# Optimization experiments

Hardware: AMD Instinct MI355X
Metric: run time of the kernel (lower is better)

## Reference

```python
import jax, jax.numpy as jnp
import numpy as np

N_HEADS = 16
HEAD_SIZE = 64
N_EMBD = N_HEADS * HEAD_SIZE  # 1024
B, T = 4, 2048


def setup_inputs() -> dict:
    key = jax.random.key(0)
    kx, kq, kk, kv, kp = jax.random.split(key, 5)
    s = 1.0 / np.sqrt(N_EMBD)
    return {
        "x": jax.random.normal(kx, (B, T, N_EMBD), dtype=jnp.float32),
        "Wq": jax.random.normal(kq, (N_EMBD, N_HEADS * HEAD_SIZE), dtype=jnp.float32) * s,
        "Wk": jax.random.normal(kk, (N_EMBD, N_HEADS * HEAD_SIZE), dtype=jnp.float32) * s,
        "Wv": jax.random.normal(kv, (N_EMBD, N_HEADS * HEAD_SIZE), dtype=jnp.float32) * s,
        "Wp": jax.random.normal(kp, (N_HEADS * HEAD_SIZE, N_EMBD), dtype=jnp.float32) * s,
    }


def reference(x, Wq, Wk, Wv, Wp):
    Bb, Tt, C = x.shape
    H, hs = N_HEADS, HEAD_SIZE
    # QKV projections (no bias), split heads: (B, H, T, hs)
    q = (x @ Wq).reshape(Bb, Tt, H, hs).transpose(0, 2, 1, 3)
    k = (x @ Wk).reshape(Bb, Tt, H, hs).transpose(0, 2, 1, 3)
    v = (x @ Wv).reshape(Bb, Tt, H, hs).transpose(0, 2, 1, 3)
    scores = jnp.einsum("bhqd,bhkd->bhqk", q, k) / np.sqrt(hs).astype(np.float32)
    causal = jnp.tril(jnp.ones((Tt, Tt), dtype=bool))
    scores = jnp.where(causal, scores, -jnp.inf)
    attn = jax.nn.softmax(scores, axis=-1)  # dropout p=0 -> identity
    o = jnp.einsum("bhqk,bhkd->bhqd", attn, v)  # (B, H, T, hs)
    # Faithfully replicate torch's view/transpose/view sequence:
    o = o.reshape(Bb, Tt, H * hs)          # raw reshape of (B,H,T,hs) buffer
    o = jnp.swapaxes(o, 1, 2)               # (B, H*hs, T)
    o = o.reshape(Bb, Tt, H * hs)           # contiguous().view
    return o @ Wp
```

## Files before the change

### kernel.cpp

```cpp
#include <hip/hip_runtime.h>

typedef unsigned short ush;
typedef unsigned int u32;
typedef __attribute__((ext_vector_type(4))) float f32x4;
typedef __attribute__((ext_vector_type(2))) u32 u32x2;
typedef __attribute__((ext_vector_type(8))) short short8;
typedef __attribute__((ext_vector_type(8))) ush ushx8;
typedef __attribute__((ext_vector_type(4))) ush ushx4;

#define GAS __attribute__((address_space(1)))
#define LAS __attribute__((address_space(3)))

__device__ __forceinline__ void gl_lds16(const void* g, void* l) {
  __builtin_amdgcn_global_load_lds((const GAS void*)g, (LAS void*)l, 16, 0, 0);
}

__device__ __forceinline__ ush f2bf(float f) {
  union { float f; unsigned int u; } x; x.f = f;
  unsigned int r = x.u + 0x7fffu + ((x.u >> 16) & 1u);
  return (ush)(r >> 16);
}
__device__ __forceinline__ u32 fbits(float f) {
  union { float f; u32 u; } x; x.f = f; return x.u;
}

#define NEG_BIG (-1.0e4f)
#define SCL 0.18033688f

__device__ __forceinline__ int kkey(int row) { return ((row & 3) + (row >> 2)) & 3; }

__global__ __launch_bounds__(256) void k_prep(
    const float* __restrict__ X, const float* __restrict__ W0,
    const float* __restrict__ W1, const float* __restrict__ W2,
    const float* __restrict__ W3, ush* __restrict__ Xb, ush* __restrict__ Wt) {
  __shared__ ush Ts[64][72];
  const int bx = blockIdx.x;
  if (bx < 4096) {
    int idx = bx * 256 + threadIdx.x;
    int base = idx * 8;
    f32x4 a = *(const f32x4*)(X + base);
    f32x4 b = *(const f32x4*)(X + base + 4);
    ushx8 o;
#pragma unroll
    for (int q = 0; q < 4; ++q) { o[q] = f2bf(a[q]); o[4 + q] = f2bf(b[q]); }
    *(ushx8*)(Xb + base) = o;
    return;
  }
  const int bid = bx - 4096;
  const int z = bid >> 8;
  const int k0 = (bid & 15) * 64, n0 = ((bid >> 4) & 15) * 64;
  const float* W = (z == 0) ? W0 : (z == 1) ? W1 : (z == 2) ? W2 : W3;
  ush* Ot = Wt + (size_t)z * 1048576;
  const int rr = threadIdx.x >> 4, cc = threadIdx.x & 15;
#pragma unroll
  for (int i = 0; i < 4; ++i) {
    int row = i * 16 + rr;
    f32x4 v = *(const f32x4*)(W + (size_t)(k0 + row) * 1024 + n0 + cc * 4);
#pragma unroll
    for (int q = 0; q < 4; ++q) Ts[row][cc * 4 + q] = f2bf(v[q]);
  }
  __syncthreads();
#pragma unroll
  for (int i = 0; i < 4; ++i) {
    int n = i * 16 + rr;
    ushx4 o;
#pragma unroll
    for (int q = 0; q < 4; ++q) o[q] = Ts[cc * 4 + q][n];
    *(ushx4*)(Ot + (size_t)(n0 + n) * 1024 + k0 + cc * 4) = o;
  }
}

__global__ __launch_bounds__(512, 2) void k_gemm_qkv(
    const ush* __restrict__ X, const ush* __restrict__ Wt,
    ush* __restrict__ QKV, ush* __restrict__ Vtg) {
  __shared__ __align__(16) ush sm[36864];
  const int tid = threadIdx.x;
  const int w = tid >> 6, l = tid & 63, lr = l & 15, lg = l >> 4;
  const int wm = w >> 2, wn = w & 3;
  const int mt = blockIdx.x, nt = blockIdx.y;
  const int which = nt >> 3, n0 = (nt & 7) * 128;
  const ush* Ag = X + (size_t)mt * 256 * 1024;
  const ush* Bg = Wt + (size_t)which * 1048576 + (size_t)n0 * 1024;
  int aoff[2], boff;
  {
#pragma unroll
    for (int it = 0; it < 2; ++it) {
      int ch = it * 512 + tid, row = ch >> 2, g = ch & 3;
      aoff[it] = row * 1024 + ((g ^ kkey(row)) << 3);
    }
    int row = tid >> 2, g = tid & 3;
    boff = row * 1024 + ((g ^ kkey(row)) << 3);
  }
  f32x4 acc[8][2] = {};

  auto issueS = [&](int kt, int st) {
    const ush* Asrc = Ag + kt * 32;
    const ush* Bsrc = Bg + kt * 32;
    ush* base = sm + st * 12288;
#pragma unroll
    for (int it = 0; it < 2; ++it)
      gl_lds16(Asrc + aoff[it], base + ((size_t)it * 512 + tid) * 8);
    gl_lds16(Bsrc + boff, base + 8192 + (size_t)tid * 8);
  };

  issueS(0, 0);
  issueS(1, 1);
  int st = 0, st2 = 2;
  for (int t = 0; t < 32; ++t) {
    if (t < 31) {
      asm volatile("s_waitcnt vmcnt(3)" ::: "memory");
    } else {
      asm volatile("s_waitcnt vmcnt(0)" ::: "memory");
    }
    __syncthreads();
    if (t + 2 < 32) issueS(t + 2, st2);
    const ush* Ab = sm + st * 12288;
    const ush* Bb = sm + st * 12288 + 8192;
    short8 fb[2];
#pragma unroll
    for (int ni = 0; ni < 2; ++ni) {
      int row = wn * 32 + ni * 16 + lr;
      fb[ni] = *(const short8*)(Bb + row * 32 + ((lg ^ kkey(row)) << 3));
    }
#pragma unroll
    for (int qm = 0; qm < 4; ++qm) {
      short8 fa[2];
#pragma unroll
      for (int m2 = 0; m2 < 2; ++m2) {
        int row = wm * 128 + (qm * 2 + m2) * 16 + lr;
        fa[m2] = *(const short8*)(Ab + row * 32 + ((lg ^ kkey(row)) << 3));
      }
      __builtin_amdgcn_s_setprio(1);
#pragma unroll
      for (int m2 = 0; m2 < 2; ++m2)
#pragma unroll
        for (int ni = 0; ni < 2; ++ni)
          acc[qm * 2 + m2][ni] = __builtin_amdgcn_mfma_f32_16x16x32_bf16(
              fa[m2], fb[ni], acc[qm * 2 + m2][ni], 0, 0, 0);
      __builtin_amdgcn_s_setprio(0);
    }
    st = (st == 2) ? 0 : st + 1;
    st2 = (st2 == 2) ? 0 : st2 + 1;
  }
  __syncthreads();
  const float oscale = (which == 0) ? SCL : 1.0f;
  ush* Ct = sm;
#pragma unroll
  for (int mi = 0; mi < 8; ++mi)
#pragma unroll
    for (int ni = 0; ni < 2; ++ni)
#pragma unroll
      for (int j = 0; j < 4; ++j)
        Ct[(wm * 128 + mi * 16 + lg * 4 + j) * 128 + wn * 32 + ni * 16 + lr] =
            f2bf(acc[mi][ni][j] * oscale);
  __syncthreads();
  const int m0 = mt * 256, b = m0 >> 11, t0 = m0 & 2047, h0 = n0 >> 6;
  if (which == 2) {
    const int cc = tid & 127, rq = tid >> 7;
    const int hsel = cc >> 6, d = cc & 63;
    ush* dst = Vtg + (size_t)(b * 16 + h0 + hsel) * 131072 + (size_t)d * 2048 +
               t0 + rq * 64;
#pragma unroll
    for (int ch = 0; ch < 8; ++ch) {
      ushx8 v;
#pragma unroll
      for (int k = 0; k < 8; ++k) v[k] = Ct[(rq * 64 + ch * 8 + k) * 128 + cc];
      *(ushx8*)(dst + ch * 8) = v;
    }
  } else {
    ush* Om = QKV + (size_t)which * 8388608;
#pragma unroll
    for (int it = 0; it < 8; ++it) {
      int c = it * 512 + tid;
      int hsel = c >> 11;
      int cc = c & 2047;
      int r = cc >> 3;
      int c8 = (cc & 7) * 8;
      ushx8 v = *(const ushx8*)(Ct + r * 128 + hsel * 64 + c8);
      *(ushx8*)(Om + ((size_t)(b * 16 + h0 + hsel) * 2048 + t0 + r) * 64 + c8) = v;
    }
  }
}

__global__ __launch_bounds__(256) void k_attn(
    const ush* __restrict__ Q, const ush* __restrict__ K,
    const ush* __restrict__ Vg, ush* __restrict__ O) {
  __shared__ __align__(16) ush Ks[2][4096];
  __shared__ __align__(16) ush Vs[2][4096];
  __shared__ __align__(16) ush Pl[8][1024];
  const int lid = blockIdx.x + 16 * blockIdx.y;
  const int qta = (lid >> 3) & 15;
  const int bh  = ((lid >> 7) << 3) | (lid & 7);
  const int qtb = 31 - qta;
  const size_t hb = (size_t)bh * (2048 * 64);
  const ush* Qh = Q + hb;
  const ush* Kh = K + hb;
  const ush* Vh = Vg + hb;
  const int tid = threadIdx.x, w = tid >> 6, l = tid & 63, lr = l & 15, lg = l >> 4;
  const int q0a = qta * 64 + w * 16, q0b = qtb * 64 + w * 16;

  short8 qfa[2], qfb[2];
#pragma unroll
  for (int s = 0; s < 2; ++s) {
    qfa[s] = *(const short8*)(Qh + (size_t)(q0a + lr) * 64 + s * 32 + lg * 8);
    qfb[s] = *(const short8*)(Qh + (size_t)(q0b + lr) * 64 + s * 32 + lg * 8);
  }
  f32x4 acca[4] = {}, accb[4] = {};
  float la = 0.f, lb = 0.f;

  int koff[2], voff[2];
#pragma unroll
  for (int it = 0; it < 2; ++it) {
    int ch = it * 256 + tid;
    int r = ch >> 3, g = ch & 7;
    koff[it] = r * 64 + ((g ^ (r & 7)) << 3);
    int keyv = ((r & 7) + (r >> 3)) & 7;
    voff[it] = r * 2048 + ((g ^ keyv) << 3);
  }
  auto issueStage = [&](int c, int buf) {
#pragma unroll
    for (int it = 0; it < 2; ++it) {
      int ch = it * 256 + tid;
      gl_lds16(Kh + (size_t)c * 4096 + koff[it], &Ks[buf][ch * 8]);
      gl_lds16(Vh + c * 64 + voff[it], &Vs[buf][ch * 8]);
    }
  };

  auto ctile = [&](const ush* Kc, const ush* Vc, const short8* qf,
                   f32x4* acc, float& lsum, bool diag, ush* PlW) {
    f32x4 sf[4] = {};
    __builtin_amdgcn_s_setprio(1);
#pragma unroll
    for (int s = 0; s < 2; ++s)
#pragma unroll
      for (int f = 0; f < 4; ++f) {
        int kv = f * 16 + lr;
        short8 kf = *(const short8*)(Kc + kv * 64 + (((s * 4 + lg) ^ (kv & 7)) << 3));
        sf[f] = __builtin_amdgcn_mfma_f32_16x16x32_bf16(kf, qf[s], sf[f], 0, 0, 0);
      }
    __builtin_amdgcn_s_setprio(0);
#pragma unroll
    for (int f = 0; f < 4; ++f)
#pragma unroll
      for (int j = 0; j < 4; ++j) {
        float vv = sf[f][j];
        if (diag && (f * 16 + lg * 4 + j) > (w * 16 + lr)) vv = NEG_BIG;
        sf[f][j] = __builtin_amdgcn_exp2f(vv);
      }
#pragma unroll
    for (int f = 0; f < 4; ++f)
      lsum += (sf[f][0] + sf[f][1]) + (sf[f][2] + sf[f][3]);
#pragma unroll
    for (int f = 0; f < 4; ++f) {
      u32 lo = (fbits(sf[f][1]) & 0xffff0000u) | (fbits(sf[f][0]) >> 16);
      u32 hi = (fbits(sf[f][3]) & 0xffff0000u) | (fbits(sf[f][2]) >> 16);
      int chunk = f * 2 + (lg >> 1);
      u32x2 pk; pk[0] = lo; pk[1] = hi;
      *(u32x2*)(PlW + lr * 64 + ((chunk ^ (lr & 7)) << 3) + (lg & 1) * 4) = pk;
    }
    __builtin_amdgcn_s_setprio(1);
#pragma unroll
    for (int s = 0; s < 2; ++s) {
      short8 pf = *(const short8*)(PlW + lr * 64 + (((s * 4 + lg) ^ (lr & 7)) << 3));
#pragma unroll
      for (int db = 0; db < 4; ++db) {
        int dv = db * 16 + lr;
        int keyv = ((dv & 7) + (dv >> 3)) & 7;
        short8 vf = *(const short8*)(Vc + dv * 64 + (((s * 4 + lg) ^ keyv) << 3));
        acc[db] = __builtin_amdgcn_mfma_f32_16x16x32_bf16(pf, vf, acc[db], 0, 0, 0);
      }
    }
    __builtin_amdgcn_s_setprio(0);
  };

  issueStage(0, 0);
  int cur = 0;
  for (int c = 0; c <= qtb; ++c) {
    asm volatile("s_waitcnt vmcnt(0)" ::: "memory");
    __syncthreads();
    if (c < qtb) issueStage(c + 1, cur ^ 1);
    const ush* Kc = Ks[cur];
    const ush* Vc = Vs[cur];
    if (c <= qta) ctile(Kc, Vc, qfa, acca, la, c == qta, Pl[w]);
    ctile(Kc, Vc, qfb, accb, lb, c == qtb, Pl[4 + w]);
    cur ^= 1;
  }

  la += __shfl_xor(la, 16); la += __shfl_xor(la, 32);
  lb += __shfl_xor(lb, 16); lb += __shfl_xor(lb, 32);
  float ra = __builtin_amdgcn_rcpf(la);
  float rb = __builtin_amdgcn_rcpf(lb);
  float ia[4], ib[4];
#pragma unroll
  for (int j = 0; j < 4; ++j) {
    ia[j] = __shfl(ra, lg * 4 + j);
    ib[j] = __shfl(rb, lg * 4 + j);
  }
  ush* Oh = O + hb;
#pragma unroll
  for (int db = 0; db < 4; ++db)
#pragma unroll
    for (int j = 0; j < 4; ++j) {
      Oh[(size_t)(q0a + lg * 4 + j) * 64 + db * 16 + lr] = f2bf(acca[db][j] * ia[j]);
      Oh[(size_t)(q0b + lg * 4 + j) * 64 + db * 16 + lr] = f2bf(accb[db][j] * ib[j]);
    }
}

__global__ __launch_bounds__(256) void k_gather(const ush* __restrict__ Ob, ush* __restrict__ Mb) {
  __shared__ ush Ls[2][128][68];
  const int jh = blockIdx.x, tau = blockIdx.y, b = blockIdx.z;
  const int tid = threadIdx.x;
#pragma unroll
  for (int it = 0; it < 8; ++it) {
    int c = it * 256 + tid;
    int r = c >> 3, d8 = (c & 7) * 8;
    int esel = r >> 7, jlow = r & 127;
    ushx8 v = *(const ushx8*)(Ob +
        ((size_t)(b * 16 + jh + esel * 8) * 2048 + jlow * 16 + tau) * 64 + d8);
    *(ushx8*)(&Ls[esel][jlow][d8]) = v;
  }
  __syncthreads();
  const int wv = tid >> 6, l = tid & 63;
  const int e = wv >> 1, jhalf = wv & 1, d = l;
  ush* Mrow = Mb + (size_t)b * 2097152 +
              (size_t)(128 * tau + 2 * d + e) * 1024 + jh * 128 + jhalf * 64;
#pragma unroll
  for (int ch = 0; ch < 8; ++ch) {
    ushx8 v;
#pragma unroll
    for (int k = 0; k < 8; ++k) v[k] = Ls[e][jhalf * 64 + ch * 8 + k][d];
    *(ushx8*)(Mrow + ch * 8) = v;
  }
}

__global__ __launch_bounds__(512, 2) void k_gemm_out(
    const ush* __restrict__ A, const ush* __restrict__ Bt, float* __restrict__ Out) {
  __shared__ __align__(16) ush sm[36864];
  const int tid = threadIdx.x;
  const int w = tid >> 6, l = tid & 63, lr = l & 15, lg = l >> 4;
  const int wm = w >> 2, wn = w & 3;
  const int mt = blockIdx.x, nt = blockIdx.y;
  const int n0 = nt * 128;
  const ush* Ag = A + (size_t)mt * 256 * 1024;
  const ush* Bg = Bt + (size_t)n0 * 1024;
  int aoff[2], boff;
  {
#pragma unroll
    for (int it = 0; it < 2; ++it) {
      int ch = it * 512 + tid, row = ch >> 2, g = ch & 3;
      aoff[it] = row * 1024 + ((g ^ kkey(row)) << 3);
    }
    int row = tid >> 2, g = tid & 3;
    boff = row * 1024 + ((g ^ kkey(row)) << 3);
  }
  f32x4 acc[8][2] = {};

  auto issueS = [&](int kt, int st) {
    const ush* Asrc = Ag + kt * 32;
    const ush* Bsrc = Bg + kt * 32;
    ush* base = sm + st * 12288;
#pragma unroll
    for (int it = 0; it < 2; ++it)
      gl_lds16(Asrc + aoff[it], base + ((size_t)it * 512 + tid) * 8);
    gl_lds16(Bsrc + boff, base + 8192 + (size_t)tid * 8);
  };

  issueS(0, 0);
  issueS(1, 1);
  int st = 0, st2 = 2;
  for (int t = 0; t < 32; ++t) {
    if (t < 31) {
      asm volatile("s_waitcnt vmcnt(3)" ::: "memory");
    } else {
      asm volatile("s_waitcnt vmcnt(0)" ::: "memory");
    }
    __syncthreads();
    if (t + 2 < 32) issueS(t + 2, st2);
    const ush* Ab = sm + st * 12288;
    const ush* Bb = sm + st * 12288 + 8192;
    short8 fb[2];
#pragma unroll
    for (int ni = 0; ni < 2; ++ni) {
      int row = wn * 32 + ni * 16 + lr;
      fb[ni] = *(const short8*)(Bb + row * 32 + ((lg ^ kkey(row)) << 3));
    }
#pragma unroll
    for (int qm = 0; qm < 4; ++qm) {
      short8 fa[2];
#pragma unroll
      for (int m2 = 0; m2 < 2; ++m2) {
        int row = wm * 128 + (qm * 2 + m2) * 16 + lr;
        fa[m2] = *(const short8*)(Ab + row * 32 + ((lg ^ kkey(row)) << 3));
      }
      __builtin_amdgcn_s_setprio(1);
#pragma unroll
      for (int m2 = 0; m2 < 2; ++m2)
#pragma unroll
        for (int ni = 0; ni < 2; ++ni)
          acc[qm * 2 + m2][ni] = __builtin_amdgcn_mfma_f32_16x16x32_bf16(
              fa[m2], fb[ni], acc[qm * 2 + m2][ni], 0, 0, 0);
      __builtin_amdgcn_s_setprio(0);
    }
    st = (st == 2) ? 0 : st + 1;
    st2 = (st2 == 2) ? 0 : st2 + 1;
  }
  const int m0 = mt * 256;
#pragma unroll
  for (int mi = 0; mi < 8; ++mi)
#pragma unroll
    for (int ni = 0; ni < 2; ++ni)
#pragma unroll
      for (int j = 0; j < 4; ++j)
        Out[(size_t)(m0 + wm * 128 + mi * 16 + lg * 4 + j) * 1024 +
            n0 + wn * 32 + ni * 16 + lr] = acc[mi][ni][j];
}

extern "C" void kernel_launch(void* const* d_in, const int* in_sizes, int n_in,
                              void* d_out, int out_size, void* d_ws, size_t ws_size,
                              hipStream_t stream) {
  const float* x  = (const float*)d_in[0];
  const float* wq = (const float*)d_in[1];
  const float* wk = (const float*)d_in[2];
  const float* wv = (const float*)d_in[3];
  const float* wp = (const float*)d_in[4];
  float* out = (float*)d_out;
  char* ws = (char*)d_ws;
  ush* xb  = (ush*)ws;
  ush* wt  = (ush*)(ws + 16777216);
  ush* qkv = (ush*)(ws + 25165824);
  ush* vtg = (ush*)(ws + 75497472);
  ush* ob  = qkv;
  ush* mb  = xb;

  k_prep<<<dim3(5120), 256, 0, stream>>>(x, wq, wk, wv, wp, xb, wt);
  k_gemm_qkv<<<dim3(32, 24), 512, 0, stream>>>(xb, wt, qkv, vtg);
  k_attn<<<dim3(16, 64), 256, 0, stream>>>(qkv, qkv + 8388608, vtg, ob);
  k_gather<<<dim3(8, 16, 4), 256, 0, stream>>>(ob, mb);
  k_gemm_out<<<dim3(32, 8), 512, 0, stream>>>(mb, wt + 3145728, out);
}
```

Baseline: 189.7 us.

## Double per-block query tile to 128 rows and hoist K/V fragment loads

Each attention block now covers two 128-row query tiles (paired causally) instead of two 64-row tiles, and each wave handles two 16-row sub-tiles per tile. K and V fragments are loaded from LDS once per chunk into registers and reused across all four sub-tile computations, which cuts LDS reads and global K/V traffic per query row. The grid is halved and launch_bounds now asks for 2 blocks per CU. In exchange, register pressure rises (hoisted kf/vf and doubled accumulators), there are fewer blocks, and the larger tiles give coarser load balance.

```diff
diff --git a/kernel.cpp b/kernel.cpp
--- a/kernel.cpp
+++ b/kernel.cpp
@@ -182,31 +182,37 @@
   }
 }
 
-__global__ __launch_bounds__(256) void k_attn(
+__global__ __launch_bounds__(256, 2) void k_attn(
     const ush* __restrict__ Q, const ush* __restrict__ K,
     const ush* __restrict__ Vg, ush* __restrict__ O) {
   __shared__ __align__(16) ush Ks[2][4096];
   __shared__ __align__(16) ush Vs[2][4096];
-  __shared__ __align__(16) ush Pl[8][1024];
-  const int lid = blockIdx.x + 16 * blockIdx.y;
-  const int qta = (lid >> 3) & 15;
-  const int bh  = ((lid >> 7) << 3) | (lid & 7);
-  const int qtb = 31 - qta;
+  __shared__ __align__(16) ush Pl[16][1024];
+  const int lid = blockIdx.x + 8 * blockIdx.y;
+  const int qta = (lid >> 3) & 7;
+  const int bh  = ((lid >> 6) << 3) | (lid & 7);
+  const int qtb = 15 - qta;
   const size_t hb = (size_t)bh * (2048 * 64);
   const ush* Qh = Q + hb;
   const ush* Kh = K + hb;
   const ush* Vh = Vg + hb;
   const int tid = threadIdx.x, w = tid >> 6, l = tid & 63, lr = l & 15, lg = l >> 4;
-  const int q0a = qta * 64 + w * 16, q0b = qtb * 64 + w * 16;
-
-  short8 qfa[2], qfb[2];
-#pragma unroll
-  for (int s = 0; s < 2; ++s) {
-    qfa[s] = *(const short8*)(Qh + (size_t)(q0a + lr) * 64 + s * 32 + lg * 8);
-    qfb[s] = *(const short8*)(Qh + (size_t)(q0b + lr) * 64 + s * 32 + lg * 8);
-  }
-  f32x4 acca[4] = {}, accb[4] = {};
-  float la = 0.f, lb = 0.f;
+  const int qbA = qta * 128 + w * 32, qbB = qtb * 128 + w * 32;
+
+  short8 qfA[2][2], qfB[2][2];
+#pragma unroll
+  for (int sub = 0; sub < 2; ++sub)
+#pragma unroll
+    for (int s = 0; s < 2; ++s) {
+      qfA[sub][s] = *(const short8*)(Qh + (size_t)(qbA + sub * 16 + lr) * 64 + s * 32 + lg * 8);
+      qfB[sub][s] = *(const short8*)(Qh + (size_t)(qbB + sub * 16 + lr) * 64 + s * 32 + lg * 8);
+    }
+  f32x4 accA[2][4] = {}, accB[2][4] = {};
+  float lA[2] = {0.f, 0.f}, lB[2] = {0.f, 0.f};
+
+  const int dA0 = 2 * qta + ((2 * w + 0) >> 2), dA1 = 2 * qta + ((2 * w + 1) >> 2);
+  const int dB0 = 2 * qtb + ((2 * w + 0) >> 2), dB1 = 2 * qtb + ((2 * w + 1) >> 2);
+  const int qo0 = ((2 * w + 0) & 3) * 16, qo1 = ((2 * w + 1) & 3) * 16;
 
   int koff[2], voff[2];
 #pragma unroll
@@ -226,25 +232,23 @@
     }
   };
 
-  auto ctile = [&](const ush* Kc, const ush* Vc, const short8* qf,
-                   f32x4* acc, float& lsum, bool diag, ush* PlW) {
+  short8 kf[2][4], vf[2][4];
+  auto csub = [&](const short8* qf, f32x4* acc, float& lsum, bool diag,
+                  int qoff, ush* PlW) {
     f32x4 sf[4] = {};
     __builtin_amdgcn_s_setprio(1);
 #pragma unroll
     for (int s = 0; s < 2; ++s)
 #pragma unroll
-      for (int f = 0; f < 4; ++f) {
-        int kv = f * 16 + lr;
-        short8 kf = *(const short8*)(Kc + kv * 64 + (((s * 4 + lg) ^ (kv & 7)) << 3));
-        sf[f] = __builtin_amdgcn_mfma_f32_16x16x32_bf16(kf, qf[s], sf[f], 0, 0, 0);
-      }
+      for (int f = 0; f < 4; ++f)
+        sf[f] = __builtin_amdgcn_mfma_f32_16x16x32_bf16(kf[s][f], qf[s], sf[f], 0, 0, 0);
     __builtin_amdgcn_s_setprio(0);
 #pragma unroll
     for (int f = 0; f < 4; ++f)
 #pragma unroll
       for (int j = 0; j < 4; ++j) {
         float vv = sf[f][j];
-        if (diag && (f * 16 + lg * 4 + j) > (w * 16 + lr)) vv = NEG_BIG;
+        if (diag && (f * 16 + lg * 4 + j) > (qoff + lr)) vv = NEG_BIG;
         sf[f][j] = __builtin_amdgcn_exp2f(vv);
       }
 #pragma unroll
@@ -263,47 +267,62 @@
     for (int s = 0; s < 2; ++s) {
       short8 pf = *(const short8*)(PlW + lr * 64 + (((s * 4 + lg) ^ (lr & 7)) << 3));
 #pragma unroll
+      for (int db = 0; db < 4; ++db)
+        acc[db] = __builtin_amdgcn_mfma_f32_16x16x32_bf16(pf, vf[s][db], acc[db], 0, 0, 0);
+    }
+    __builtin_amdgcn_s_setprio(0);
+  };
+
+  issueStage(0, 0);
+  int cur = 0;
+  const int cmax = 2 * qtb + 2;
+  for (int c = 0; c < cmax; ++c) {
+    asm volatile("s_waitcnt vmcnt(0)" ::: "memory");
+    __syncthreads();
+    if (c + 1 < cmax) issueStage(c + 1, cur ^ 1);
+    const ush* Kc = Ks[cur];
+    const ush* Vc = Vs[cur];
+#pragma unroll
+    for (int s = 0; s < 2; ++s)
+#pragma unroll
+      for (int f = 0; f < 4; ++f)
+        kf[s][f] = *(const short8*)(Kc + (f * 16 + lr) * 64 + (((s * 4 + lg) ^ (lr & 7)) << 3));
+#pragma unroll
+    for (int s = 0; s < 2; ++s)
+#pragma unroll
       for (int db = 0; db < 4; ++db) {
         int dv = db * 16 + lr;
         int keyv = ((dv & 7) + (dv >> 3)) & 7;
-        short8 vf = *(const short8*)(Vc + dv * 64 + (((s * 4 + lg) ^ keyv) << 3));
-        acc[db] = __builtin_amdgcn_mfma_f32_16x16x32_bf16(pf, vf, acc[db], 0, 0, 0);
+        vf[s][db] = *(const short8*)(Vc + dv * 64 + (((s * 4 + lg) ^ keyv) << 3));
       }
-    }
-    __builtin_amdgcn_s_setprio(0);
-  };
-
-  issueStage(0, 0);
-  int cur = 0;
-  for (int c = 0; c <= qtb; ++c) {
-    asm volatile("s_waitcnt vmcnt(0)" ::: "memory");
-    __syncthreads();
-    if (c < qtb) issueStage(c + 1, cur ^ 1);
-    const ush* Kc = Ks[cur];
-    const ush* Vc = Vs[cur];
-    if (c <= qta) ctile(Kc, Vc, qfa, acca, la, c == qta, Pl[w]);
-    ctile(Kc, Vc, qfb, accb, lb, c == qtb, Pl[4 + w]);
+    if (c <= dA0) csub(qfA[0], accA[0], lA[0], c == dA0, qo0, Pl[(w << 2) | 0]);
+    if (c <= dA1) csub(qfA[1], accA[1], lA[1], c == dA1, qo1, Pl[(w << 2) | 1]);
+    if (c <= dB0) csub(qfB[0], accB[0], lB[0], c == dB0, qo0, Pl[(w << 2) | 2]);
+    if (c <= dB1) csub(qfB[1], accB[1], lB[1], c == dB1, qo1, Pl[(w << 2) | 3]);
     cur ^= 1;
   }
 
-  la += __shfl_xor(la, 16); la += __shfl_xor(la, 32);
-  lb += __shfl_xor(lb, 16); lb += __shfl_xor(lb, 32);
-  float ra = __builtin_amdgcn_rcpf(la);
-  float rb = __builtin_amdgcn_rcpf(lb);
-  float ia[4], ib[4];
-#pragma unroll
-  for (int j = 0; j < 4; ++j) {
-    ia[j] = __shfl(ra, lg * 4 + j);
-    ib[j] = __shfl(rb, lg * 4 + j);
-  }
   ush* Oh = O + hb;
 #pragma unroll
-  for (int db = 0; db < 4; ++db)
+  for (int sub = 0; sub < 2; ++sub) {
+    float la = lA[sub], lb = lB[sub];
+    la += __shfl_xor(la, 16); la += __shfl_xor(la, 32);
+    lb += __shfl_xor(lb, 16); lb += __shfl_xor(lb, 32);
+    float ra = __builtin_amdgcn_rcpf(la);
+    float rb = __builtin_amdgcn_rcpf(lb);
 #pragma unroll
     for (int j = 0; j < 4; ++j) {
-      Oh[(size_t)(q0a + lg * 4 + j) * 64 + db * 16 + lr] = f2bf(acca[db][j] * ia[j]);
-      Oh[(size_t)(q0b + lg * 4 + j) * 64 + db * 16 + lr] = f2bf(accb[db][j] * ib[j]);
-    }
+      float ia = __shfl(ra, lg * 4 + j);
+      float ib = __shfl(rb, lg * 4 + j);
+#pragma unroll
+      for (int db = 0; db < 4; ++db) {
+        Oh[(size_t)(qbA + sub * 16 + lg * 4 + j) * 64 + db * 16 + lr] =
+            f2bf(accA[sub][db][j] * ia);
+        Oh[(size_t)(qbB + sub * 16 + lg * 4 + j) * 64 + db * 16 + lr] =
+            f2bf(accB[sub][db][j] * ib);
+      }
+    }
+  }
 }
 
 __global__ __launch_bounds__(256) void k_gather(const ush* __restrict__ Ob, ush* __restrict__ Mb) {
@@ -434,7 +453,7 @@
 
   k_prep<<<dim3(5120), 256, 0, stream>>>(x, wq, wk, wv, wp, xb, wt);
   k_gemm_qkv<<<dim3(32, 24), 512, 0, stream>>>(xb, wt, qkv, vtg);
-  k_attn<<<dim3(16, 64), 256, 0, stream>>>(qkv, qkv + 8388608, vtg, ob);
+  k_attn<<<dim3(8, 64), 256, 0, stream>>>(qkv, qkv + 8388608, vtg, ob);
   k_gather<<<dim3(8, 16, 4), 256, 0, stream>>>(ob, mb);
   k_gemm_out<<<dim3(32, 8), 512, 0, stream>>>(mb, wt + 3145728, out);
 }
```

Result: faster. 183.3 us (-3.4%).
